# Kernel optimization log

Hardware: AMD Instinct MI355X
Metric: run time of the kernel (lower is better)

The kernel has to match this reference:

```python
import jax, jax.numpy as jnp
import numpy as np

B, T, D = 2, 1024, 2048
H, KV, DH = 16, 4, 128
REP = H // KV
LAMBDA_INIT = 0.8 - 0.6 * float(np.exp(-0.3 * 1))  # layer_idx=2
ROPE_BASE = 10000.0
GN_EPS = 1e-5


def _rope(x, pos):
    # x: (B, h, T, DH), pos: (T,) int
    inv = 1.0 / (ROPE_BASE ** (jnp.arange(0, DH, 2, dtype=jnp.float32) / DH))
    freqs = pos.astype(jnp.float32)[:, None] * inv[None, :]          # (T, DH/2)
    cos = jnp.cos(freqs)[None, None, :, :].astype(x.dtype)
    sin = jnp.sin(freqs)[None, None, :, :].astype(x.dtype)
    x1, x2 = x[..., ::2], x[..., 1::2]
    o1 = x1 * cos - x2 * sin
    o2 = x1 * sin + x2 * cos
    return jnp.stack([o1, o2], axis=-1).reshape(x.shape)


def setup_inputs() -> dict:
    key = jax.random.key(0)
    ks = jax.random.split(key, 10)
    s = 0.02
    return {
        "x": jax.random.normal(ks[0], (B, T, D), jnp.float32),
        "Wq": jax.random.normal(ks[1], (2 * H * DH, D), jnp.float32) * s,
        "Wk": jax.random.normal(ks[2], (2 * KV * DH, D), jnp.float32) * s,
        "Wv": jax.random.normal(ks[3], (2 * KV * DH, D), jnp.float32) * s,
        "Wo": jax.random.normal(ks[4], (D, 2 * H * DH), jnp.float32) * s,
        "lambda_q1": jax.random.normal(ks[5], (DH,), jnp.float32) * 0.1,
        "lambda_k1": jax.random.normal(ks[6], (DH,), jnp.float32) * 0.1,
        "lambda_q2": jax.random.normal(ks[7], (DH,), jnp.float32) * 0.1,
        "lambda_k2": jax.random.normal(ks[8], (DH,), jnp.float32) * 0.1,
        "gn_weight": jnp.ones((2 * H * DH,), jnp.float32),
        "gn_bias": jnp.zeros((2 * H * DH,), jnp.float32),
        "pos": jnp.arange(T, dtype=jnp.int64 if jax.config.jax_enable_x64 else jnp.int32),
    }


def reference(x, Wq, Wk, Wv, Wo, lambda_q1, lambda_k1, lambda_q2, lambda_k2, gn_weight, gn_bias, pos):
    b, t, _ = x.shape
    # projections
    q = (x @ Wq.T).reshape(b, t, H, 2, DH)        # two query streams per head
    k = (x @ Wk.T).reshape(b, t, KV, 2, DH)       # two key streams per kv-head
    v = (x @ Wv.T).reshape(b, t, KV, 2 * DH)      # single value, 2*Dh per kv-head
    q1 = q[..., 0, :].transpose(0, 2, 1, 3)       # (B,H,T,DH)
    q2 = q[..., 1, :].transpose(0, 2, 1, 3)
    k1 = k[..., 0, :].transpose(0, 2, 1, 3)       # (B,KV,T,DH)
    k2 = k[..., 1, :].transpose(0, 2, 1, 3)
    v = v.transpose(0, 2, 1, 3)                   # (B,KV,T,2DH)
    # RoPE on all Q/K streams
    q1, q2 = _rope(q1, pos), _rope(q2, pos)
    k1, k2 = _rope(k1, pos), _rope(k2, pos)
    # GQA repeat kv heads
    k1 = jnp.repeat(k1, REP, axis=1)
    k2 = jnp.repeat(k2, REP, axis=1)
    vr = jnp.repeat(v, REP, axis=1)               # (B,H,T,2DH)
    scale = DH ** -0.5
    neg = jnp.asarray(-jnp.inf, x.dtype)
    causal = jnp.tril(jnp.ones((t, t), bool))
    s1 = jnp.einsum("bhqd,bhkd->bhqk", q1, k1) * scale
    s2 = jnp.einsum("bhqd,bhkd->bhqk", q2, k2) * scale
    a1 = jax.nn.softmax(jnp.where(causal, s1, neg), axis=-1)
    a2 = jax.nn.softmax(jnp.where(causal, s2, neg), axis=-1)
    lam = (jnp.exp(jnp.sum(lambda_q1 * lambda_k1))
           - jnp.exp(jnp.sum(lambda_q2 * lambda_k2))
           + LAMBDA_INIT)
    attn = a1 - lam * a2
    out = jnp.einsum("bhqk,bhkd->bhqd", attn, vr)  # (B,H,T,2DH)
    # GroupNorm: num_groups=H over 2*H*DH channels == per-head norm over 2*DH
    o = out.transpose(0, 2, 1, 3)                  # (B,T,H,2DH)
    mu = jnp.mean(o, axis=-1, keepdims=True)
    var = jnp.var(o, axis=-1, keepdims=True)
    o = (o - mu) * jax.lax.rsqrt(var + GN_EPS)
    o = o * gn_weight.reshape(H, 2 * DH) + gn_bias.reshape(H, 2 * DH)
    o = o * (1.0 - LAMBDA_INIT)
    o = o.reshape(b, t, 2 * H * DH)
    return o @ Wo.T
```

## Files before the change

### kernel.cpp

```cpp
#include <hip/hip_runtime.h>
#include <hip/hip_bf16.h>

#define BB 2
#define TT 1024
#define DD 2048
#define NH 16
#define NKV 4
#define DHD 128
#define DVV 256

#define LAMBDA_INIT 0.35550906759096927f
#define ONE_MINUS_LI 0.6444909324090307f
#define QSCALE (0.08838834764831845f * 1.4426950408889634f)

typedef __attribute__((ext_vector_type(8))) short bf16x8;
typedef __attribute__((ext_vector_type(4))) float f32x4;

static __device__ __forceinline__ short f2bf_s(float x) {
    __hip_bfloat16 h = __float2bfloat16(x);
    return __builtin_bit_cast(short, h);
}
static __device__ __forceinline__ float bfu2f(unsigned short u) {
    union { float f; unsigned int u32; } x;
    x.u32 = ((unsigned int)u) << 16;
    return x.f;
}

#define GLOAD_LDS16(g, l)                                                      \
    __builtin_amdgcn_global_load_lds(                                          \
        (const __attribute__((address_space(1))) unsigned int*)(g),            \
        (__attribute__((address_space(3))) unsigned int*)(l), 16, 0, 0)

__global__ void cast_bf16(const float* __restrict__ in, __hip_bfloat16* __restrict__ out, int n4) {
    int i = blockIdx.x * blockDim.x + threadIdx.x;
    if (i >= n4) return;
    const float4 v = reinterpret_cast<const float4*>(in)[i];
    union { ushort4 u; __hip_bfloat16 b[4]; } o;
    o.b[0] = __float2bfloat16(v.x);
    o.b[1] = __float2bfloat16(v.y);
    o.b[2] = __float2bfloat16(v.z);
    o.b[3] = __float2bfloat16(v.w);
    reinterpret_cast<ushort4*>(out)[i] = o.u;
}

__global__ __launch_bounds__(256) void gemm128_db(const __hip_bfloat16* __restrict__ A,
                                                  const __hip_bfloat16* __restrict__ Bm,
                                                  float* __restrict__ C,
                                                  int M, int N, int sK, int kLen) {
    __shared__ ushort As[2][128 * 32];
    __shared__ ushort Bs[2][128 * 32];
    const int tid = threadIdx.x;
    const int lane = tid & 63, wid = tid >> 6;
    const int lo = lane & 15, hi = lane >> 4;
    const int wr = wid >> 1, wc = wid & 1;
    const int m0 = blockIdx.y * 128, n0 = blockIdx.x * 128;
    const int kOff = blockIdx.z * kLen;

    const ushort* gA = (const ushort*)A;
    const ushort* gB = (const ushort*)Bm;
    C += (size_t)blockIdx.z * M * N;

    const int c0row = tid >> 2;
    const int c0col = (tid & 3) << 3;

    auto STAGE = [&](int buf, int kg) {
#pragma unroll
        for (int q = 0; q < 2; ++q) {
            const int row = q * 64 + c0row;
            const int idx = q * 256 + tid;
            GLOAD_LDS16(gA + (size_t)(m0 + row) * sK + kg + c0col, &As[buf][idx << 3]);
            GLOAD_LDS16(gB + (size_t)(n0 + row) * sK + kg + c0col, &Bs[buf][idx << 3]);
        }
    };

    f32x4 acc[4][4];
#pragma unroll
    for (int mi = 0; mi < 4; ++mi)
#pragma unroll
        for (int ni = 0; ni < 4; ++ni) acc[mi][ni] = (f32x4){0.f, 0.f, 0.f, 0.f};

    STAGE(0, kOff);
    const int nt = kLen >> 5;
    for (int t = 0; t < nt; ++t) {
        __syncthreads();
        if (t + 1 < nt) STAGE((t + 1) & 1, kOff + ((t + 1) << 5));
        const ushort* as = &As[t & 1][0];
        const ushort* bs = &Bs[t & 1][0];
        bf16x8 af[4], bfr[4];
#pragma unroll
        for (int mi = 0; mi < 4; ++mi)
            af[mi] = *reinterpret_cast<const bf16x8*>(&as[(wr * 64 + mi * 16 + lo) * 32 + hi * 8]);
#pragma unroll
        for (int ni = 0; ni < 4; ++ni)
            bfr[ni] = *reinterpret_cast<const bf16x8*>(&bs[(wc * 64 + ni * 16 + lo) * 32 + hi * 8]);
#pragma unroll
        for (int mi = 0; mi < 4; ++mi)
#pragma unroll
            for (int ni = 0; ni < 4; ++ni)
                acc[mi][ni] = __builtin_amdgcn_mfma_f32_16x16x32_bf16(af[mi], bfr[ni], acc[mi][ni], 0, 0, 0);
    }
#pragma unroll
    for (int mi = 0; mi < 4; ++mi)
#pragma unroll
        for (int ni = 0; ni < 4; ++ni)
#pragma unroll
            for (int r = 0; r < 4; ++r)
                C[(size_t)(m0 + wr * 64 + mi * 16 + hi * 4 + r) * N + (n0 + wc * 64 + ni * 16 + lo)] =
                    acc[mi][ni][r];
}

__global__ void addf4(const float* __restrict__ p, float* __restrict__ out, int n4) {
    int i = blockIdx.x * blockDim.x + threadIdx.x;
    if (i >= n4) return;
    const float4 a = reinterpret_cast<const float4*>(p)[i];
    const float4 b = reinterpret_cast<const float4*>(p)[i + n4];
    float4 o;
    o.x = a.x + b.x; o.y = a.y + b.y; o.z = a.z + b.z; o.w = a.w + b.w;
    reinterpret_cast<float4*>(out)[i] = o;
}

__global__ void rope_qk(const float* __restrict__ in, int stride, int col_base, int nheads, int hshift,
                        const int* __restrict__ pos, __hip_bfloat16* __restrict__ out, float scale) {
    int idx = blockIdx.x * blockDim.x + threadIdx.x;
    int total = BB * TT * nheads * 2 * 64;
    if (idx >= total) return;
    int d2 = idx & 63;
    int rest = idx >> 6;
    int e = rest & 1;
    int rest2 = rest >> 1;
    int head = rest2 & (nheads - 1);
    int bt = rest2 >> hshift;
    int t = bt & (TT - 1);
    int b = bt >> 10;

    const float* src = in + (size_t)bt * stride + col_base + head * 256 + e * 128 + 2 * d2;
    float x1 = src[0], x2 = src[1];
    float inv = expf(-(float)d2 * (2.0f / 128.0f) * 9.210340371976184f);
    float fr = (float)pos[t] * inv;
    float sn, cs;
    sincosf(fr, &sn, &cs);
    float o1 = (x1 * cs - x2 * sn) * scale;
    float o2 = (x1 * sn + x2 * cs) * scale;
    __hip_bfloat16* dst = out + ((((size_t)e * BB + b) * nheads + head) * TT + t) * DHD + 2 * d2;
    dst[0] = __float2bfloat16(o1);
    dst[1] = __float2bfloat16(o2);
}

__global__ __launch_bounds__(256) void vtrans(const float* __restrict__ in, __hip_bfloat16* __restrict__ out) {
    __shared__ float tle[64][65];
    const int t0 = blockIdx.x * 64;
    const int z = blockIdx.y;
    const int dv0 = (z & 3) * 64;
    const int kvi = (z >> 2) & 3;
    const int b = z >> 4;
    const int tid = threadIdx.x;
    const int rt = tid >> 6, ct = tid & 63;
#pragma unroll
    for (int p = 0; p < 16; ++p) {
        const int ti = p * 4 + rt;
        tle[ti][ct] = in[(size_t)(b * TT + t0 + ti) * 6144 + 5120 + kvi * 256 + dv0 + ct];
    }
    __syncthreads();
#pragma unroll
    for (int p = 0; p < 16; ++p) {
        const int dv = p * 4 + rt;
        out[((size_t)(b * NKV + kvi) * DVV + dv0 + dv) * TT + t0 + ct] = __float2bfloat16(tle[ct][dv]);
    }
}

__global__ void lam_k(const float* __restrict__ lq1, const float* __restrict__ lk1,
                      const float* __restrict__ lq2, const float* __restrict__ lk2,
                      float* __restrict__ lam) {
    int l = threadIdx.x;
    float s1 = lq1[l] * lk1[l] + lq1[l + 64] * lk1[l + 64];
    float s2 = lq2[l] * lk2[l] + lq2[l + 64] * lk2[l + 64];
#pragma unroll
    for (int mm = 1; mm < 64; mm <<= 1) {
        s1 += __shfl_xor(s1, mm, 64);
        s2 += __shfl_xor(s2, mm, 64);
    }
    if (l == 0) lam[0] = expf(s1) - expf(s2) + LAMBDA_INIT;
}

__global__ __launch_bounds__(256) void attn_fused(const __hip_bfloat16* __restrict__ qb,
                                                  const __hip_bfloat16* __restrict__ kb,
                                                  const __hip_bfloat16* __restrict__ vtb,
                                                  __hip_bfloat16* __restrict__ Obuf) {
    const int tid = threadIdx.x;
    const int wid = tid >> 6;
    const int lane = tid & 63;
    const int lo = lane & 15, hi = lane >> 4;
    const int qt = (int)gridDim.x - 1 - blockIdx.x;
    const int bh = blockIdx.y;
    const int e = blockIdx.z;
    const int b = bh >> 4, h = bh & 15;
    const int kv = h >> 2;

    const ushort* qp = (const ushort*)qb + (((size_t)e * BB + b) * NH + h) * (size_t)TT * DHD;
    const ushort* kp = (const ushort*)kb + (((size_t)e * BB + b) * NKV + kv) * (size_t)TT * DHD;
    const ushort* vp = (const ushort*)vtb + ((size_t)b * NKV + kv) * (size_t)DVV * TT;

    const int q0 = qt * 64 + wid * 16;

    __shared__ ushort Ks[64 * 128];
    __shared__ ushort Vs[256 * 64];

    bf16x8 qf[4];
#pragma unroll
    for (int kk = 0; kk < 4; ++kk)
        qf[kk] = *reinterpret_cast<const bf16x8*>(qp + (size_t)(q0 + lo) * DHD + kk * 32 + hi * 8);

    f32x4 O[16];
#pragma unroll
    for (int nc = 0; nc < 16; ++nc) O[nc] = (f32x4){0.f, 0.f, 0.f, 0.f};
    float m = -3e38f, l = 0.f;

    const int nkt = qt + 1;
    for (int kt = 0; kt < nkt; ++kt) {
        const int kbase = kt * 64;
#pragma unroll
        for (int p2 = 0; p2 < 4; ++p2) {
            const int idx = p2 * 256 + tid;
            const int row = idx >> 4, c = idx & 15;
            const int cp = c ^ ((row & 3) | ((row >> 1) & 4));
            GLOAD_LDS16(kp + (((size_t)(kbase + row)) << 7) + (cp << 3), &Ks[idx << 3]);
        }
#pragma unroll
        for (int p2 = 0; p2 < 8; ++p2) {
            const int idx = p2 * 256 + tid;
            const int dv = idx >> 3, c = idx & 7;
            const int cp = c ^ (dv & 7);
            GLOAD_LDS16(vp + (size_t)dv * TT + kbase + (cp << 3), &Vs[idx << 3]);
        }
        __syncthreads();

        f32x4 s[4];
#pragma unroll
        for (int n = 0; n < 4; ++n) s[n] = (f32x4){0.f, 0.f, 0.f, 0.f};
        __builtin_amdgcn_s_setprio(1);
#pragma unroll
        for (int n = 0; n < 4; ++n) {
            const int R = ((n >> 1) << 5) + ((lo >> 2) << 3) + ((n & 1) << 2) + (lo & 3);
            const int swz = ((R & 3) | ((R >> 1) & 4)) << 4;
#pragma unroll
            for (int kk = 0; kk < 4; ++kk) {
                bf16x8 kf = *reinterpret_cast<const bf16x8*>(
                    (const char*)Ks + R * 256 + ((kk * 64 + hi * 16) ^ swz));
                s[n] = __builtin_amdgcn_mfma_f32_16x16x32_bf16(kf, qf[kk], s[n], 0, 0, 0);
            }
        }
        __builtin_amdgcn_s_setprio(0);

        if (kt == nkt - 1) {
#pragma unroll
            for (int n = 0; n < 4; ++n) {
                const int kb0 = kbase + ((n >> 1) << 5) + ((n & 1) << 2) + hi * 8;
#pragma unroll
                for (int r = 0; r < 4; ++r)
                    if (kb0 + r > q0 + lo) s[n][r] = -3e38f;
            }
        }
        float tm = s[0][0];
#pragma unroll
        for (int n = 0; n < 4; ++n)
#pragma unroll
            for (int r = 0; r < 4; ++r) tm = fmaxf(tm, s[n][r]);
        tm = fmaxf(tm, __shfl_xor(tm, 16, 64));
        tm = fmaxf(tm, __shfl_xor(tm, 32, 64));
        if (!__all(tm <= m + 11.f)) {
            const float mn = fmaxf(m, tm);
            const float resc = __builtin_amdgcn_exp2f(m - mn);
            m = mn;
            l *= resc;
            float ro[4];
#pragma unroll
            for (int r = 0; r < 4; ++r) ro[r] = __shfl(resc, hi * 4 + r, 64);
#pragma unroll
            for (int nc = 0; nc < 16; ++nc)
#pragma unroll
                for (int r = 0; r < 4; ++r) O[nc][r] *= ro[r];
        }
        float rs = 0.f;
#pragma unroll
        for (int n = 0; n < 4; ++n)
#pragma unroll
            for (int r = 0; r < 4; ++r) {
                const float p = __builtin_amdgcn_exp2f(s[n][r] - m);
                s[n][r] = p;
                rs += p;
            }
        rs += __shfl_xor(rs, 16, 64);
        rs += __shfl_xor(rs, 32, 64);
        l += rs;
        bf16x8 pf[2];
#pragma unroll
        for (int n = 0; n < 4; ++n)
#pragma unroll
            for (int r = 0; r < 4; ++r) pf[n >> 1][(n & 1) * 4 + r] = f2bf_s(s[n][r]);
        __builtin_amdgcn_s_setprio(1);
#pragma unroll
        for (int nc = 0; nc < 16; ++nc) {
            const int vrow = (nc * 16 + lo) * 128;
            const int vswz = (lo & 7) << 4;
#pragma unroll
            for (int ks = 0; ks < 2; ++ks) {
                bf16x8 vf = *reinterpret_cast<const bf16x8*>(
                    (const char*)Vs + vrow + ((ks * 64 + hi * 16) ^ vswz));
                O[nc] = __builtin_amdgcn_mfma_f32_16x16x32_bf16(pf[ks], vf, O[nc], 0, 0, 0);
            }
        }
        __builtin_amdgcn_s_setprio(0);
        __syncthreads();
    }
    const float invl = 1.0f / l;
    float io[4];
#pragma unroll
    for (int r = 0; r < 4; ++r) io[r] = __shfl(invl, hi * 4 + r, 64);
    ushort* op = (ushort*)Obuf + (((size_t)e * BB + b) * NH + h) * (size_t)TT * DVV;
#pragma unroll
    for (int nc = 0; nc < 16; ++nc)
#pragma unroll
        for (int r = 0; r < 4; ++r)
            op[(size_t)(q0 + hi * 4 + r) * DVV + nc * 16 + lo] = (ushort)f2bf_s(O[nc][r] * io[r]);
}

__global__ __launch_bounds__(256) void gn_combine(const __hip_bfloat16* __restrict__ Obuf,
                                                  const float* __restrict__ lamp,
                                                  const float* __restrict__ gw, const float* __restrict__ gb,
                                                  __hip_bfloat16* __restrict__ obf) {
    const int wid = threadIdx.x >> 6, lane = threadIdx.x & 63;
    const int rid = blockIdx.x * 4 + wid;
    const int t = rid & (TT - 1);
    const int h = (rid >> 10) & 15;
    const int b = rid >> 14;
    const float lam = lamp[0];
    const size_t E = (size_t)BB * NH * TT * DVV;
    const ushort* o1p = (const ushort*)Obuf + (size_t)rid * DVV + lane * 4;
    const ushort4 u1 = *reinterpret_cast<const ushort4*>(o1p);
    const ushort4 u2 = *reinterpret_cast<const ushort4*>(o1p + E);
    float val[4];
    val[0] = bfu2f(u1.x) - lam * bfu2f(u2.x);
    val[1] = bfu2f(u1.y) - lam * bfu2f(u2.y);
    val[2] = bfu2f(u1.z) - lam * bfu2f(u2.z);
    val[3] = bfu2f(u1.w) - lam * bfu2f(u2.w);
    float sum = val[0] + val[1] + val[2] + val[3];
    float ss = val[0] * val[0] + val[1] * val[1] + val[2] * val[2] + val[3] * val[3];
#pragma unroll
    for (int mm = 1; mm < 64; mm <<= 1) {
        sum += __shfl_xor(sum, mm, 64);
        ss += __shfl_xor(ss, mm, 64);
    }
    const float mean = sum * (1.0f / 256.0f);
    const float var = ss * (1.0f / 256.0f) - mean * mean;
    const float rs = rsqrtf(var + 1e-5f);
    const int c = h * 256 + lane * 4;
    const float4 gwv = *reinterpret_cast<const float4*>(gw + c);
    const float4 gbv = *reinterpret_cast<const float4*>(gb + c);
    union { ushort4 u; short s[4]; } o;
    o.s[0] = f2bf_s(((val[0] - mean) * rs * gwv.x + gbv.x) * ONE_MINUS_LI);
    o.s[1] = f2bf_s(((val[1] - mean) * rs * gwv.y + gbv.y) * ONE_MINUS_LI);
    o.s[2] = f2bf_s(((val[2] - mean) * rs * gwv.z + gbv.z) * ONE_MINUS_LI);
    o.s[3] = f2bf_s(((val[3] - mean) * rs * gwv.w + gbv.w) * ONE_MINUS_LI);
    const int bt = b * TT + t;
    *reinterpret_cast<ushort4*>((ushort*)obf + (size_t)bt * 4096 + c) = o.u;
}

extern "C" void kernel_launch(void* const* d_in, const int* in_sizes, int n_in,
                              void* d_out, int out_size, void* d_ws, size_t ws_size,
                              hipStream_t stream) {
    const float* x = (const float*)d_in[0];
    const float* Wq = (const float*)d_in[1];
    const float* Wk = (const float*)d_in[2];
    const float* Wv = (const float*)d_in[3];
    const float* Wo = (const float*)d_in[4];
    const float* lq1 = (const float*)d_in[5];
    const float* lk1 = (const float*)d_in[6];
    const float* lq2 = (const float*)d_in[7];
    const float* lk2 = (const float*)d_in[8];
    const float* gw = (const float*)d_in[9];
    const float* gb = (const float*)d_in[10];
    const int* pos = (const int*)d_in[11];

    char* ws = (char*)d_ws;
    const size_t oXB = 0;
    const size_t oWQKV = 8388608;
    const size_t oWO = 33554432;
    const size_t oQKVF = 50331648;
    const size_t oOB = 50331648;
    const size_t oPK = 50331648;
    const size_t oLAM = 83886080;
    const size_t oQB = 100663296;
    const size_t oKB = 117440512;
    const size_t oVT = 121634816;
    const size_t oON = 125829120;

    auto bfp = [&](size_t off) { return (__hip_bfloat16*)(ws + off); };
    auto fp = [&](size_t off) { return (float*)(ws + off); };

    int n;
    n = BB * TT * DD / 4;
    cast_bf16<<<dim3((n + 255) / 256), 256, 0, stream>>>(x, bfp(oXB), n);
    n = 4096 * 2048 / 4;
    cast_bf16<<<dim3((n + 255) / 256), 256, 0, stream>>>(Wq, bfp(oWQKV), n);
    n = 1024 * 2048 / 4;
    cast_bf16<<<dim3((n + 255) / 256), 256, 0, stream>>>(Wk, bfp(oWQKV + (size_t)4096 * 2048 * 2), n);
    cast_bf16<<<dim3((n + 255) / 256), 256, 0, stream>>>(Wv, bfp(oWQKV + (size_t)5120 * 2048 * 2), n);
    n = 2048 * 4096 / 4;
    cast_bf16<<<dim3((n + 255) / 256), 256, 0, stream>>>(Wo, bfp(oWO), n);

    gemm128_db<<<dim3(6144 / 128, 2048 / 128, 1), 256, 0, stream>>>(
        bfp(oXB), bfp(oWQKV), fp(oQKVF), 2048, 6144, 2048, 2048);

    n = BB * TT * NH * 2 * 64;
    rope_qk<<<dim3((n + 255) / 256), 256, 0, stream>>>(fp(oQKVF), 6144, 0, NH, 4, pos, bfp(oQB), QSCALE);
    n = BB * TT * NKV * 2 * 64;
    rope_qk<<<dim3((n + 255) / 256), 256, 0, stream>>>(fp(oQKVF), 6144, 4096, NKV, 2, pos, bfp(oKB), 1.0f);
    vtrans<<<dim3(TT / 64, BB * NKV * 4), 256, 0, stream>>>(fp(oQKVF), bfp(oVT));

    lam_k<<<dim3(1), 64, 0, stream>>>(lq1, lk1, lq2, lk2, fp(oLAM));

    attn_fused<<<dim3(TT / 64, BB * NH, 2), 256, 0, stream>>>(bfp(oQB), bfp(oKB), bfp(oVT), bfp(oOB));

    gn_combine<<<dim3(BB * NH * TT / 4), 256, 0, stream>>>(bfp(oOB), fp(oLAM), gw, gb, bfp(oON));

    gemm128_db<<<dim3(2048 / 128, 2048 / 128, 2), 256, 0, stream>>>(
        bfp(oON), bfp(oWO), fp(oPK), 2048, 2048, 4096, 2048);
    n = 2048 * 2048 / 4;
    addf4<<<dim3((n + 255) / 256), 256, 0, stream>>>(fp(oPK), (float*)d_out, n);
}
```

Before: 438.3 us.

## Pair causal query tiles per attention block and merge cast/rope launches

Each attention block now handles two query tiles, a high one (15-pi) and a low one (pi). It walks the K/V tiles once and reuses each loaded tile for both, which balances causal work across blocks and halves the K/V global loads per query. Launch bounds are set to 2 blocks per CU, and the grid shrinks to 8 blocks along x. The five cast launches are merged into one kernel, and the two rope launches into one. In exchange the attention kernel uses more registers (two O accumulators of 64 floats each), which risks spills or lower occupancy.

New measurement: 564.0 us. +28.7%, slower.

```diff
diff --git a/kernel.cpp b/kernel.cpp
--- a/kernel.cpp
+++ b/kernel.cpp
@@ -31,16 +31,27 @@
         (const __attribute__((address_space(1))) unsigned int*)(g),            \
         (__attribute__((address_space(3))) unsigned int*)(l), 16, 0, 0)
 
-__global__ void cast_bf16(const float* __restrict__ in, __hip_bfloat16* __restrict__ out, int n4) {
-    int i = blockIdx.x * blockDim.x + threadIdx.x;
-    if (i >= n4) return;
-    const float4 v = reinterpret_cast<const float4*>(in)[i];
+__global__ void cast_all(const float* __restrict__ x, const float* __restrict__ wq,
+                         const float* __restrict__ wk, const float* __restrict__ wv,
+                         const float* __restrict__ wo,
+                         __hip_bfloat16* __restrict__ dx, __hip_bfloat16* __restrict__ dwqkv,
+                         __hip_bfloat16* __restrict__ dwo) {
+    const int i = blockIdx.x * 256 + threadIdx.x;
+    const float* src;
+    ushort4* dst;
+    int s4;
+    if (i < 1048576) { src = x; dst = (ushort4*)dx; s4 = i; }
+    else if (i < 3145728) { src = wq; dst = (ushort4*)dwqkv; s4 = i - 1048576; }
+    else if (i < 3670016) { src = wk; dst = (ushort4*)dwqkv + 2097152; s4 = i - 3145728; }
+    else if (i < 4194304) { src = wv; dst = (ushort4*)dwqkv + 2621440; s4 = i - 3670016; }
+    else { src = wo; dst = (ushort4*)dwo; s4 = i - 4194304; }
+    const float4 v = reinterpret_cast<const float4*>(src)[s4];
     union { ushort4 u; __hip_bfloat16 b[4]; } o;
     o.b[0] = __float2bfloat16(v.x);
     o.b[1] = __float2bfloat16(v.y);
     o.b[2] = __float2bfloat16(v.z);
     o.b[3] = __float2bfloat16(v.w);
-    reinterpret_cast<ushort4*>(out)[i] = o.u;
+    dst[s4] = o.u;
 }
 
 __global__ __launch_bounds__(256) void gemm128_db(const __hip_bfloat16* __restrict__ A,
@@ -119,13 +130,17 @@
     reinterpret_cast<float4*>(out)[i] = o;
 }
 
-__global__ void rope_qk(const float* __restrict__ in, int stride, int col_base, int nheads, int hshift,
-                        const int* __restrict__ pos, __hip_bfloat16* __restrict__ out, float scale) {
+__global__ void rope_all(const float* __restrict__ in, const int* __restrict__ pos,
+                         __hip_bfloat16* __restrict__ qb, __hip_bfloat16* __restrict__ kb) {
     int idx = blockIdx.x * blockDim.x + threadIdx.x;
-    int total = BB * TT * nheads * 2 * 64;
-    if (idx >= total) return;
-    int d2 = idx & 63;
-    int rest = idx >> 6;
+    int nheads, hshift, col_base, li;
+    float scale;
+    __hip_bfloat16* outp;
+    if (idx < 4194304) { nheads = 16; hshift = 4; col_base = 0; outp = qb; scale = QSCALE; li = idx; }
+    else { nheads = 4; hshift = 2; col_base = 4096; outp = kb; scale = 1.0f; li = idx - 4194304; }
+
+    int d2 = li & 63;
+    int rest = li >> 6;
     int e = rest & 1;
     int rest2 = rest >> 1;
     int head = rest2 & (nheads - 1);
@@ -133,7 +148,7 @@
     int t = bt & (TT - 1);
     int b = bt >> 10;
 
-    const float* src = in + (size_t)bt * stride + col_base + head * 256 + e * 128 + 2 * d2;
+    const float* src = in + (size_t)bt * 6144 + col_base + head * 256 + e * 128 + 2 * d2;
     float x1 = src[0], x2 = src[1];
     float inv = expf(-(float)d2 * (2.0f / 128.0f) * 9.210340371976184f);
     float fr = (float)pos[t] * inv;
@@ -141,7 +156,7 @@
     sincosf(fr, &sn, &cs);
     float o1 = (x1 * cs - x2 * sn) * scale;
     float o2 = (x1 * sn + x2 * cs) * scale;
-    __hip_bfloat16* dst = out + ((((size_t)e * BB + b) * nheads + head) * TT + t) * DHD + 2 * d2;
+    __hip_bfloat16* dst = outp + ((((size_t)e * BB + b) * nheads + head) * TT + t) * DHD + 2 * d2;
     dst[0] = __float2bfloat16(o1);
     dst[1] = __float2bfloat16(o2);
 }
@@ -182,15 +197,87 @@
     if (l == 0) lam[0] = expf(s1) - expf(s2) + LAMBDA_INIT;
 }
 
-__global__ __launch_bounds__(256) void attn_fused(const __hip_bfloat16* __restrict__ qb,
-                                                  const __hip_bfloat16* __restrict__ kb,
-                                                  const __hip_bfloat16* __restrict__ vtb,
-                                                  __hip_bfloat16* __restrict__ Obuf) {
+#define QK_TWO(SH, SL)                                                              \
+    _Pragma("unroll") for (int n = 0; n < 4; ++n) {                                 \
+        const int R = ((n >> 1) << 5) + ((lo >> 2) << 3) + ((n & 1) << 2) + (lo & 3); \
+        const int swz = ((R & 3) | ((R >> 1) & 4)) << 4;                            \
+        _Pragma("unroll") for (int kk = 0; kk < 4; ++kk) {                          \
+            bf16x8 kf = *reinterpret_cast<const bf16x8*>(                           \
+                (const char*)Ks + R * 256 + ((kk * 64 + hi * 16) ^ swz));           \
+            SH[n] = __builtin_amdgcn_mfma_f32_16x16x32_bf16(kf, qfh[kk], SH[n], 0, 0, 0); \
+            SL[n] = __builtin_amdgcn_mfma_f32_16x16x32_bf16(kf, qfl[kk], SL[n], 0, 0, 0); \
+        }                                                                           \
+    }
+
+#define QK_ONE(SH)                                                                  \
+    _Pragma("unroll") for (int n = 0; n < 4; ++n) {                                 \
+        const int R = ((n >> 1) << 5) + ((lo >> 2) << 3) + ((n & 1) << 2) + (lo & 3); \
+        const int swz = ((R & 3) | ((R >> 1) & 4)) << 4;                            \
+        _Pragma("unroll") for (int kk = 0; kk < 4; ++kk) {                          \
+            bf16x8 kf = *reinterpret_cast<const bf16x8*>(                           \
+                (const char*)Ks + R * 256 + ((kk * 64 + hi * 16) ^ swz));           \
+            SH[n] = __builtin_amdgcn_mfma_f32_16x16x32_bf16(kf, qfh[kk], SH[n], 0, 0, 0); \
+        }                                                                           \
+    }
+
+#define SM_STEP(S, M, LSUM, O, PF, ISDIAG, KB, Q0)                                  \
+    {                                                                               \
+        if (ISDIAG) {                                                               \
+            _Pragma("unroll") for (int n = 0; n < 4; ++n) {                         \
+                const int kb0 = (KB) + ((n >> 1) << 5) + ((n & 1) << 2) + hi * 8;   \
+                _Pragma("unroll") for (int r = 0; r < 4; ++r)                       \
+                    if (kb0 + r > (Q0) + lo) S[n][r] = -3e38f;                      \
+            }                                                                       \
+        }                                                                           \
+        float tm = S[0][0];                                                         \
+        _Pragma("unroll") for (int n = 0; n < 4; ++n)                               \
+            _Pragma("unroll") for (int r = 0; r < 4; ++r) tm = fmaxf(tm, S[n][r]);  \
+        tm = fmaxf(tm, __shfl_xor(tm, 16, 64));                                     \
+        tm = fmaxf(tm, __shfl_xor(tm, 32, 64));                                     \
+        if (!__all(tm <= M + 11.f)) {                                               \
+            const float mn = fmaxf(M, tm);                                          \
+            const float rsc = __builtin_amdgcn_exp2f(M - mn);                       \
+            M = mn; LSUM *= rsc;                                                    \
+            float ro[4];                                                            \
+            _Pragma("unroll") for (int r = 0; r < 4; ++r) ro[r] = __shfl(rsc, hi * 4 + r, 64); \
+            _Pragma("unroll") for (int nc = 0; nc < 16; ++nc)                       \
+                _Pragma("unroll") for (int r = 0; r < 4; ++r) O[nc][r] *= ro[r];    \
+        }                                                                           \
+        float rsum = 0.f;                                                           \
+        _Pragma("unroll") for (int n = 0; n < 4; ++n)                               \
+            _Pragma("unroll") for (int r = 0; r < 4; ++r) {                         \
+                const float p = __builtin_amdgcn_exp2f(S[n][r] - M);                \
+                S[n][r] = p; rsum += p;                                             \
+            }                                                                       \
+        rsum += __shfl_xor(rsum, 16, 64);                                           \
+        rsum += __shfl_xor(rsum, 32, 64);                                           \
+        LSUM += rsum;                                                               \
+        _Pragma("unroll") for (int n = 0; n < 4; ++n)                               \
+            _Pragma("unroll") for (int r = 0; r < 4; ++r)                           \
+                PF[n >> 1][(n & 1) * 4 + r] = f2bf_s(S[n][r]);                      \
+    }
+
+#define EPILOG(LSUM, O, Q0)                                                         \
+    {                                                                               \
+        const float invl = 1.0f / LSUM;                                             \
+        float io[4];                                                                \
+        _Pragma("unroll") for (int r = 0; r < 4; ++r) io[r] = __shfl(invl, hi * 4 + r, 64); \
+        _Pragma("unroll") for (int nc = 0; nc < 16; ++nc)                           \
+            _Pragma("unroll") for (int r = 0; r < 4; ++r)                           \
+                op[(size_t)((Q0) + hi * 4 + r) * DVV + nc * 16 + lo] =              \
+                    (ushort)f2bf_s(O[nc][r] * io[r]);                               \
+    }
+
+__global__ __launch_bounds__(256, 2) void attn_fused(const __hip_bfloat16* __restrict__ qb,
+                                                     const __hip_bfloat16* __restrict__ kb,
+                                                     const __hip_bfloat16* __restrict__ vtb,
+                                                     __hip_bfloat16* __restrict__ Obuf) {
     const int tid = threadIdx.x;
     const int wid = tid >> 6;
     const int lane = tid & 63;
     const int lo = lane & 15, hi = lane >> 4;
-    const int qt = (int)gridDim.x - 1 - blockIdx.x;
+    const int pi = blockIdx.x;
+    const int qth = 15 - pi, qtl = pi;
     const int bh = blockIdx.y;
     const int e = blockIdx.z;
     const int b = bh >> 4, h = bh & 15;
@@ -200,23 +287,29 @@
     const ushort* kp = (const ushort*)kb + (((size_t)e * BB + b) * NKV + kv) * (size_t)TT * DHD;
     const ushort* vp = (const ushort*)vtb + ((size_t)b * NKV + kv) * (size_t)DVV * TT;
 
-    const int q0 = qt * 64 + wid * 16;
+    const int q0h = qth * 64 + wid * 16;
+    const int q0l = qtl * 64 + wid * 16;
 
     __shared__ ushort Ks[64 * 128];
     __shared__ ushort Vs[256 * 64];
 
-    bf16x8 qf[4];
-#pragma unroll
-    for (int kk = 0; kk < 4; ++kk)
-        qf[kk] = *reinterpret_cast<const bf16x8*>(qp + (size_t)(q0 + lo) * DHD + kk * 32 + hi * 8);
-
-    f32x4 O[16];
-#pragma unroll
-    for (int nc = 0; nc < 16; ++nc) O[nc] = (f32x4){0.f, 0.f, 0.f, 0.f};
-    float m = -3e38f, l = 0.f;
-
-    const int nkt = qt + 1;
-    for (int kt = 0; kt < nkt; ++kt) {
+    bf16x8 qfh[4], qfl[4];
+#pragma unroll
+    for (int kk = 0; kk < 4; ++kk) {
+        qfh[kk] = *reinterpret_cast<const bf16x8*>(qp + (size_t)(q0h + lo) * DHD + kk * 32 + hi * 8);
+        qfl[kk] = *reinterpret_cast<const bf16x8*>(qp + (size_t)(q0l + lo) * DHD + kk * 32 + hi * 8);
+    }
+
+    f32x4 Oh[16], Ol[16];
+#pragma unroll
+    for (int nc = 0; nc < 16; ++nc) {
+        Oh[nc] = (f32x4){0.f, 0.f, 0.f, 0.f};
+        Ol[nc] = (f32x4){0.f, 0.f, 0.f, 0.f};
+    }
+    float mh = -3e38f, sumh = 0.f;
+    float ml = -3e38f, suml = 0.f;
+
+    for (int kt = 0; kt <= qth; ++kt) {
         const int kbase = kt * 64;
 #pragma unroll
         for (int p2 = 0; p2 < 4; ++p2) {
@@ -234,94 +327,55 @@
         }
         __syncthreads();
 
-        f32x4 s[4];
-#pragma unroll
-        for (int n = 0; n < 4; ++n) s[n] = (f32x4){0.f, 0.f, 0.f, 0.f};
+        const bool dol = (kt <= qtl);
+        f32x4 sh[4], sl[4];
+#pragma unroll
+        for (int n = 0; n < 4; ++n) {
+            sh[n] = (f32x4){0.f, 0.f, 0.f, 0.f};
+            sl[n] = (f32x4){0.f, 0.f, 0.f, 0.f};
+        }
         __builtin_amdgcn_s_setprio(1);
-#pragma unroll
-        for (int n = 0; n < 4; ++n) {
-            const int R = ((n >> 1) << 5) + ((lo >> 2) << 3) + ((n & 1) << 2) + (lo & 3);
-            const int swz = ((R & 3) | ((R >> 1) & 4)) << 4;
-#pragma unroll
-            for (int kk = 0; kk < 4; ++kk) {
-                bf16x8 kf = *reinterpret_cast<const bf16x8*>(
-                    (const char*)Ks + R * 256 + ((kk * 64 + hi * 16) ^ swz));
-                s[n] = __builtin_amdgcn_mfma_f32_16x16x32_bf16(kf, qf[kk], s[n], 0, 0, 0);
+        if (dol) { QK_TWO(sh, sl); }
+        else { QK_ONE(sh); }
+        __builtin_amdgcn_s_setprio(0);
+
+        bf16x8 pfh[2], pfl[2];
+        SM_STEP(sh, mh, sumh, Oh, pfh, kt == qth, kbase, q0h);
+        if (dol) SM_STEP(sl, ml, suml, Ol, pfl, kt == qtl, kbase, q0l);
+
+        __builtin_amdgcn_s_setprio(1);
+        if (dol) {
+#pragma unroll
+            for (int nc = 0; nc < 16; ++nc) {
+                const int vrow = (nc * 16 + lo) * 128;
+                const int vswz = (lo & 7) << 4;
+#pragma unroll
+                for (int ks = 0; ks < 2; ++ks) {
+                    bf16x8 vf = *reinterpret_cast<const bf16x8*>(
+                        (const char*)Vs + vrow + ((ks * 64 + hi * 16) ^ vswz));
+                    Oh[nc] = __builtin_amdgcn_mfma_f32_16x16x32_bf16(pfh[ks], vf, Oh[nc], 0, 0, 0);
+                    Ol[nc] = __builtin_amdgcn_mfma_f32_16x16x32_bf16(pfl[ks], vf, Ol[nc], 0, 0, 0);
+                }
             }
-        }
-        __builtin_amdgcn_s_setprio(0);
-
-        if (kt == nkt - 1) {
-#pragma unroll
-            for (int n = 0; n < 4; ++n) {
-                const int kb0 = kbase + ((n >> 1) << 5) + ((n & 1) << 2) + hi * 8;
-#pragma unroll
-                for (int r = 0; r < 4; ++r)
-                    if (kb0 + r > q0 + lo) s[n][r] = -3e38f;
-            }
-        }
-        float tm = s[0][0];
-#pragma unroll
-        for (int n = 0; n < 4; ++n)
-#pragma unroll
-            for (int r = 0; r < 4; ++r) tm = fmaxf(tm, s[n][r]);
-        tm = fmaxf(tm, __shfl_xor(tm, 16, 64));
-        tm = fmaxf(tm, __shfl_xor(tm, 32, 64));
-        if (!__all(tm <= m + 11.f)) {
-            const float mn = fmaxf(m, tm);
-            const float resc = __builtin_amdgcn_exp2f(m - mn);
-            m = mn;
-            l *= resc;
-            float ro[4];
-#pragma unroll
-            for (int r = 0; r < 4; ++r) ro[r] = __shfl(resc, hi * 4 + r, 64);
-#pragma unroll
-            for (int nc = 0; nc < 16; ++nc)
-#pragma unroll
-                for (int r = 0; r < 4; ++r) O[nc][r] *= ro[r];
-        }
-        float rs = 0.f;
-#pragma unroll
-        for (int n = 0; n < 4; ++n)
-#pragma unroll
-            for (int r = 0; r < 4; ++r) {
-                const float p = __builtin_amdgcn_exp2f(s[n][r] - m);
-                s[n][r] = p;
-                rs += p;
-            }
-        rs += __shfl_xor(rs, 16, 64);
-        rs += __shfl_xor(rs, 32, 64);
-        l += rs;
-        bf16x8 pf[2];
-#pragma unroll
-        for (int n = 0; n < 4; ++n)
-#pragma unroll
-            for (int r = 0; r < 4; ++r) pf[n >> 1][(n & 1) * 4 + r] = f2bf_s(s[n][r]);
-        __builtin_amdgcn_s_setprio(1);
-#pragma unroll
-        for (int nc = 0; nc < 16; ++nc) {
-            const int vrow = (nc * 16 + lo) * 128;
-            const int vswz = (lo & 7) << 4;
-#pragma unroll
-            for (int ks = 0; ks < 2; ++ks) {
-                bf16x8 vf = *reinterpret_cast<const bf16x8*>(
-                    (const char*)Vs + vrow + ((ks * 64 + hi * 16) ^ vswz));
-                O[nc] = __builtin_amdgcn_mfma_f32_16x16x32_bf16(pf[ks], vf, O[nc], 0, 0, 0);
+        } else {
+#pragma unroll
+            for (int nc = 0; nc < 16; ++nc) {
+                const int vrow = (nc * 16 + lo) * 128;
+                const int vswz = (lo & 7) << 4;
+#pragma unroll
+                for (int ks = 0; ks < 2; ++ks) {
+                    bf16x8 vf = *reinterpret_cast<const bf16x8*>(
+                        (const char*)Vs + vrow + ((ks * 64 + hi * 16) ^ vswz));
+                    Oh[nc] = __builtin_amdgcn_mfma_f32_16x16x32_bf16(pfh[ks], vf, Oh[nc], 0, 0, 0);
+                }
             }
         }
         __builtin_amdgcn_s_setprio(0);
         __syncthreads();
     }
-    const float invl = 1.0f / l;
-    float io[4];
-#pragma unroll
-    for (int r = 0; r < 4; ++r) io[r] = __shfl(invl, hi * 4 + r, 64);
     ushort* op = (ushort*)Obuf + (((size_t)e * BB + b) * NH + h) * (size_t)TT * DVV;
-#pragma unroll
-    for (int nc = 0; nc < 16; ++nc)
-#pragma unroll
-        for (int r = 0; r < 4; ++r)
-            op[(size_t)(q0 + hi * 4 + r) * DVV + nc * 16 + lo] = (ushort)f2bf_s(O[nc][r] * io[r]);
+    EPILOG(sumh, Oh, q0h);
+    EPILOG(suml, Ol, q0l);
 }
 
 __global__ __launch_bounds__(256) void gn_combine(const __hip_bfloat16* __restrict__ Obuf,
@@ -397,34 +451,22 @@
     auto bfp = [&](size_t off) { return (__hip_bfloat16*)(ws + off); };
     auto fp = [&](size_t off) { return (float*)(ws + off); };
 
-    int n;
-    n = BB * TT * DD / 4;
-    cast_bf16<<<dim3((n + 255) / 256), 256, 0, stream>>>(x, bfp(oXB), n);
-    n = 4096 * 2048 / 4;
-    cast_bf16<<<dim3((n + 255) / 256), 256, 0, stream>>>(Wq, bfp(oWQKV), n);
-    n = 1024 * 2048 / 4;
-    cast_bf16<<<dim3((n + 255) / 256), 256, 0, stream>>>(Wk, bfp(oWQKV + (size_t)4096 * 2048 * 2), n);
-    cast_bf16<<<dim3((n + 255) / 256), 256, 0, stream>>>(Wv, bfp(oWQKV + (size_t)5120 * 2048 * 2), n);
-    n = 2048 * 4096 / 4;
-    cast_bf16<<<dim3((n + 255) / 256), 256, 0, stream>>>(Wo, bfp(oWO), n);
+    cast_all<<<dim3(24576), 256, 0, stream>>>(x, Wq, Wk, Wv, Wo, bfp(oXB), bfp(oWQKV), bfp(oWO));
 
     gemm128_db<<<dim3(6144 / 128, 2048 / 128, 1), 256, 0, stream>>>(
         bfp(oXB), bfp(oWQKV), fp(oQKVF), 2048, 6144, 2048, 2048);
 
-    n = BB * TT * NH * 2 * 64;
-    rope_qk<<<dim3((n + 255) / 256), 256, 0, stream>>>(fp(oQKVF), 6144, 0, NH, 4, pos, bfp(oQB), QSCALE);
-    n = BB * TT * NKV * 2 * 64;
-    rope_qk<<<dim3((n + 255) / 256), 256, 0, stream>>>(fp(oQKVF), 6144, 4096, NKV, 2, pos, bfp(oKB), 1.0f);
+    rope_all<<<dim3(20480), 256, 0, stream>>>(fp(oQKVF), pos, bfp(oQB), bfp(oKB));
     vtrans<<<dim3(TT / 64, BB * NKV * 4), 256, 0, stream>>>(fp(oQKVF), bfp(oVT));
 
     lam_k<<<dim3(1), 64, 0, stream>>>(lq1, lk1, lq2, lk2, fp(oLAM));
 
-    attn_fused<<<dim3(TT / 64, BB * NH, 2), 256, 0, stream>>>(bfp(oQB), bfp(oKB), bfp(oVT), bfp(oOB));
+    attn_fused<<<dim3(8, BB * NH, 2), 256, 0, stream>>>(bfp(oQB), bfp(oKB), bfp(oVT), bfp(oOB));
 
     gn_combine<<<dim3(BB * NH * TT / 4), 256, 0, stream>>>(bfp(oOB), fp(oLAM), gw, gb, bfp(oON));
 
     gemm128_db<<<dim3(2048 / 128, 2048 / 128, 2), 256, 0, stream>>>(
         bfp(oON), bfp(oWO), fp(oPK), 2048, 2048, 4096, 2048);
-    n = 2048 * 2048 / 4;
+    int n = 2048 * 2048 / 4;
     addf4<<<dim3((n + 255) / 256), 256, 0, stream>>>(fp(oPK), (float*)d_out, n);
 }
```
